# Performance work log

Hardware: AMD Instinct MI355X
Metric: run time of the kernel (lower is better)

## Reference

```python
import jax, jax.numpy as jnp
import numpy as np


def _rot_x(a):  # a: [N], angle = theta[:,1]
    c, s = jnp.cos(a), jnp.sin(a)
    z, o = jnp.zeros_like(c), jnp.ones_like(c)
    return jnp.stack([
        jnp.stack([o, z, z, z], -1),
        jnp.stack([z, c, -s, z], -1),
        jnp.stack([z, s, c, z], -1),
        jnp.stack([z, z, z, o], -1)], axis=1)  # [N,4,4]


def _rot_y(a):  # angle = theta[:,0]
    c, s = jnp.cos(a), jnp.sin(a)
    z, o = jnp.zeros_like(c), jnp.ones_like(c)
    return jnp.stack([
        jnp.stack([c, z, s, z], -1),
        jnp.stack([z, o, z, z], -1),
        jnp.stack([-s, z, c, z], -1),
        jnp.stack([z, z, z, o], -1)], axis=1)


def _rot_z(a):  # angle = theta[:,2]
    c, s = jnp.cos(a), jnp.sin(a)
    z, o = jnp.zeros_like(c), jnp.ones_like(c)
    return jnp.stack([
        jnp.stack([c, -s, z, z], -1),
        jnp.stack([s, c, z, z], -1),
        jnp.stack([z, z, o, z], -1),
        jnp.stack([z, z, z, o], -1)], axis=1)


def _trans(th):  # th: [N,6] -> [N,3,4] affine translation matrix
    tx, ty, tz = th[:, 3], th[:, 4], th[:, 5]
    z, o = jnp.zeros_like(tx), jnp.ones_like(tx)
    return jnp.stack([
        jnp.stack([o, z, z, tx], -1),
        jnp.stack([z, o, z, ty], -1),
        jnp.stack([z, z, o, tz], -1)], axis=1)  # [N,3,4]


def _homogeneous(x_flat, J):
    # x_flat: [N, 3*J] -> [N, 4, J] homogeneous coords (joints as columns)
    N = x_flat.shape[0]
    pts = x_flat.reshape(N, J, 3).transpose(0, 2, 1)  # [N,3,J]
    ones = jnp.ones((N, 1, J), dtype=x_flat.dtype)
    return jnp.concatenate([pts, ones], axis=1)  # [N,4,J]


def va_forward(conv_input, theta):
    B, T, D = conv_input.shape
    J = D // 3
    th = theta.reshape(-1, theta.shape[-1])  # [N,6], N = B*T
    mask = (conv_input != 0.0).astype(conv_input.dtype)  # [B,T,D]

    # translation: out = Trans @ hom(x)
    hom = _homogeneous(conv_input.reshape(-1, D), J)  # [N,4,J]
    out = jnp.einsum('nij,njk->nik', _trans(th), hom)  # [N,3,J]
    out = out.transpose(0, 2, 1).reshape(B, T, D)
    out = out * mask

    # rotation: M = Rz @ Ry @ Rx
    M = jnp.einsum('nij,njk->nik', _rot_z(th[:, 2]), _rot_y(th[:, 0]))
    M = jnp.einsum('nij,njk->nik', M, _rot_x(th[:, 1]))  # [N,4,4]
    hom2 = _homogeneous(out.reshape(-1, D), J)  # [N,4,J]
    out2 = jnp.einsum('nij,njk->nik', M, hom2)  # [N,4,J]
    out2 = out2.transpose(0, 2, 1)[:, :, 0:3]  # [N,J,3]
    return out2.reshape(B, T, D)


def setup_inputs() -> dict:
    key = jax.random.key(0)
    k1, k2 = jax.random.split(key)
    conv_input = jax.random.normal(k1, (2048, 300, 75), dtype=jnp.float32)
    theta = jax.random.normal(k2, (2048, 300, 6), dtype=jnp.float32)
    return {"conv_input": conv_input, "theta": theta}


def reference(conv_input, theta):
    return va_forward(conv_input, theta)
```

## Files before the change

kernel.cpp:

```cpp
#include <hip/hip_runtime.h>


constexpr int JOINTS = 25;

__global__ __launch_bounds__(256) void va_kernel(
    const float* __restrict__ conv,
    const float* __restrict__ theta,
    float* __restrict__ out,
    int total)
{
    int idx = blockIdx.x * 256 + threadIdx.x;
    if (idx >= total) return;

    unsigned row = (unsigned)idx / JOINTS;
    unsigned j   = (unsigned)idx - row * JOINTS;

    const float* th = theta + (size_t)row * 6;
    float ay = th[0], ax = th[1], az = th[2];
    float tx = th[3], ty = th[4], tz = th[5];

    float sy = __sinf(ay), cy = __cosf(ay);
    float sx = __sinf(ax), cx = __cosf(ax);
    float sz = __sinf(az), cz = __cosf(az);

    float m00 = cz * cy;
    float m01 = -sz * cx + cz * sy * sx;
    float m02 =  sz * sx + cz * sy * cx;
    float m10 = sz * cy;
    float m11 =  cz * cx + sz * sy * sx;
    float m12 = -cz * sx + sz * sy * cx;
    float m20 = -sy;
    float m21 = cy * sx;
    float m22 = cy * cx;

    const float* p = conv + (size_t)row * 75 + j * 3;
    float x = p[0], y = p[1], z = p[2];

    float qx = (x != 0.0f) ? (x + tx) : 0.0f;
    float qy = (y != 0.0f) ? (y + ty) : 0.0f;
    float qz = (z != 0.0f) ? (z + tz) : 0.0f;

    float ox = m00 * qx + m01 * qy + m02 * qz;
    float oy = m10 * qx + m11 * qy + m12 * qz;
    float oz = m20 * qx + m21 * qy + m22 * qz;

    float* o = out + (size_t)row * 75 + j * 3;
    o[0] = ox;
    o[1] = oy;
    o[2] = oz;
}

extern "C" void kernel_launch(void* const* d_in, const int* in_sizes, int n_in,
                              void* d_out, int out_size, void* d_ws, size_t ws_size,
                              hipStream_t stream) {
    const float* conv  = (const float*)d_in[0];
    const float* theta = (const float*)d_in[1];
    float* out = (float*)d_out;

    int total = out_size / 3;
    int blocks = (total + 255) / 256;
    va_kernel<<<blocks, 256, 0, stream>>>(conv, theta, out, total);
}
```

Measured before the change: 71.14 us.

## Stage rows in LDS with float4 loads and compute rotation once per row

Each block now loads 32 rows of input into shared memory with coalesced float4 reads and writes results back with float4 stores. This replaces the strided 3-float accesses per thread. Sin/cos and the rotation matrix are computed once per row by 32 threads instead of once per joint, then broadcast through shared memory. The cost is two barriers, LDS traffic, and idle threads during the parameter phase. Handling of a partial final block relies on total4 bounds and assumes the total float count is divisible by 4.

```diff
diff --git a/kernel.cpp b/kernel.cpp
--- a/kernel.cpp
+++ b/kernel.cpp
@@ -1,63 +1,95 @@
 #include <hip/hip_runtime.h>
 
 
-constexpr int JOINTS = 25;
+constexpr int JOINTS          = 25;
+constexpr int FLOATS_PER_ROW  = 75;
+constexpr int ROWS_PER_BLOCK  = 32;
+constexpr int BLOCK           = 256;
+constexpr int FLOATS_PER_BLK  = ROWS_PER_BLOCK * FLOATS_PER_ROW;
+constexpr int VEC4_PER_BLK    = FLOATS_PER_BLK / 4;
+constexpr int TASKS_PER_BLK   = ROWS_PER_BLOCK * JOINTS;
 
-__global__ __launch_bounds__(256) void va_kernel(
-    const float* __restrict__ conv,
-    const float* __restrict__ theta,
-    float* __restrict__ out,
-    int total)
+__global__ __launch_bounds__(BLOCK) void va_kernel(
+    const float4* __restrict__ conv4,
+    const float*  __restrict__ theta,
+    float4*       __restrict__ out4,
+    int nrows)
 {
-    int idx = blockIdx.x * 256 + threadIdx.x;
-    if (idx >= total) return;
+    __shared__ float buf[FLOATS_PER_BLK];
+    __shared__ float prm[ROWS_PER_BLOCK][12];
 
-    unsigned row = (unsigned)idx / JOINTS;
-    unsigned j   = (unsigned)idx - row * JOINTS;
+    const int tid = threadIdx.x;
+    const size_t row0  = (size_t)blockIdx.x * ROWS_PER_BLOCK;
+    const size_t base4 = (size_t)blockIdx.x * VEC4_PER_BLK;
+    const size_t total4 = (size_t)nrows * FLOATS_PER_ROW / 4;
 
-    const float* th = theta + (size_t)row * 6;
-    float ay = th[0], ax = th[1], az = th[2];
-    float tx = th[3], ty = th[4], tz = th[5];
+    #pragma unroll
+    for (int i = tid; i < VEC4_PER_BLK; i += BLOCK) {
+        size_t g = base4 + i;
+        if (g < total4)
+            *reinterpret_cast<float4*>(&buf[i * 4]) = conv4[g];
+    }
 
-    float sy = __sinf(ay), cy = __cosf(ay);
-    float sx = __sinf(ax), cx = __cosf(ax);
-    float sz = __sinf(az), cz = __cosf(az);
+    if (tid < ROWS_PER_BLOCK) {
+        size_t row = row0 + tid;
+        if (row < (size_t)nrows) {
+            const float* th = theta + row * 6;
+            float ay = th[0], ax = th[1], az = th[2];
+            float tx = th[3], ty = th[4], tz = th[5];
 
-    float m00 = cz * cy;
-    float m01 = -sz * cx + cz * sy * sx;
-    float m02 =  sz * sx + cz * sy * cx;
-    float m10 = sz * cy;
-    float m11 =  cz * cx + sz * sy * sx;
-    float m12 = -cz * sx + sz * sy * cx;
-    float m20 = -sy;
-    float m21 = cy * sx;
-    float m22 = cy * cx;
+            float sy = __sinf(ay), cy = __cosf(ay);
+            float sx = __sinf(ax), cx = __cosf(ax);
+            float sz = __sinf(az), cz = __cosf(az);
 
-    const float* p = conv + (size_t)row * 75 + j * 3;
-    float x = p[0], y = p[1], z = p[2];
+            prm[tid][0] = cz * cy;
+            prm[tid][1] = -sz * cx + cz * sy * sx;
+            prm[tid][2] =  sz * sx + cz * sy * cx;
+            prm[tid][3] = sz * cy;
+            prm[tid][4] =  cz * cx + sz * sy * sx;
+            prm[tid][5] = -cz * sx + sz * sy * cx;
+            prm[tid][6] = -sy;
+            prm[tid][7] = cy * sx;
+            prm[tid][8] = cy * cx;
+            prm[tid][9]  = tx;
+            prm[tid][10] = ty;
+            prm[tid][11] = tz;
+        }
+    }
+    __syncthreads();
 
-    float qx = (x != 0.0f) ? (x + tx) : 0.0f;
-    float qy = (y != 0.0f) ? (y + ty) : 0.0f;
-    float qz = (z != 0.0f) ? (z + tz) : 0.0f;
+    #pragma unroll
+    for (int t = tid; t < TASKS_PER_BLK; t += BLOCK) {
+        int r = t / JOINTS;
+        float* p = &buf[3 * t];
+        const float* m = prm[r];
 
-    float ox = m00 * qx + m01 * qy + m02 * qz;
-    float oy = m10 * qx + m11 * qy + m12 * qz;
-    float oz = m20 * qx + m21 * qy + m22 * qz;
+        float x = p[0], y = p[1], z = p[2];
+        float qx = (x != 0.0f) ? (x + m[9])  : 0.0f;
+        float qy = (y != 0.0f) ? (y + m[10]) : 0.0f;
+        float qz = (z != 0.0f) ? (z + m[11]) : 0.0f;
 
-    float* o = out + (size_t)row * 75 + j * 3;
-    o[0] = ox;
-    o[1] = oy;
-    o[2] = oz;
+        p[0] = m[0] * qx + m[1] * qy + m[2] * qz;
+        p[1] = m[3] * qx + m[4] * qy + m[5] * qz;
+        p[2] = m[6] * qx + m[7] * qy + m[8] * qz;
+    }
+    __syncthreads();
+
+    #pragma unroll
+    for (int i = tid; i < VEC4_PER_BLK; i += BLOCK) {
+        size_t g = base4 + i;
+        if (g < total4)
+            out4[g] = *reinterpret_cast<const float4*>(&buf[i * 4]);
+    }
 }
 
 extern "C" void kernel_launch(void* const* d_in, const int* in_sizes, int n_in,
                               void* d_out, int out_size, void* d_ws, size_t ws_size,
                               hipStream_t stream) {
-    const float* conv  = (const float*)d_in[0];
-    const float* theta = (const float*)d_in[1];
-    float* out = (float*)d_out;
+    const float4* conv4 = (const float4*)d_in[0];
+    const float*  theta = (const float*)d_in[1];
+    float4* out4 = (float4*)d_out;
 
-    int total = out_size / 3;
-    int blocks = (total + 255) / 256;
-    va_kernel<<<blocks, 256, 0, stream>>>(conv, theta, out, total);
+    int nrows  = out_size / FLOATS_PER_ROW;
+    int blocks = (nrows + ROWS_PER_BLOCK - 1) / ROWS_PER_BLOCK;
+    va_kernel<<<blocks, BLOCK, 0, stream>>>(conv4, theta, out4, nrows);
 }
```

Measured after the change: 77.91 us. +9.5%, slower.

## Vectorize to float4 per thread with wave shuffles for cross-joint neighbors

Applied to the files above, without the earlier changes.

Each thread now handles four consecutive output floats, loaded and stored as one 16-byte nontemporal vector. Neighbouring values needed to complete xyz triplets come from adjacent lanes via shuffles, with boundary lanes falling back to scalar loads. This replaces the stride-3 scalar accesses with fully coalesced vector traffic. The cost is that each thread computes up to two rotation matrices (six sincos) because its four floats can span two rows, plus extra select logic. The launch also assumes the element count divides evenly into blocks of 1024 floats and drops the bounds check.

```diff
diff --git a/kernel.cpp b/kernel.cpp
--- a/kernel.cpp
+++ b/kernel.cpp
@@ -1,53 +1,101 @@
 #include <hip/hip_runtime.h>
 
 
-constexpr int JOINTS = 25;
+typedef float f32x4 __attribute__((ext_vector_type(4)));
 
-__global__ __launch_bounds__(256) void va_kernel(
+constexpr int BLOCK = 256;
+
+__global__ __launch_bounds__(BLOCK) void va_kernel(
     const float* __restrict__ conv,
     const float* __restrict__ theta,
     float* __restrict__ out,
-    int total)
+    int F)
 {
-    int idx = blockIdx.x * 256 + threadIdx.x;
-    if (idx >= total) return;
+    int q = blockIdx.x * BLOCK + threadIdx.x;
+    int g = q << 2;
 
-    unsigned row = (unsigned)idx / JOINTS;
-    unsigned j   = (unsigned)idx - row * JOINTS;
+    f32x4 A = __builtin_nontemporal_load((const f32x4*)conv + q);
 
-    const float* th = theta + (size_t)row * 6;
-    float ay = th[0], ax = th[1], az = th[2];
-    float tx = th[3], ty = th[4], tz = th[5];
+    int lane = threadIdx.x & 63;
 
-    float sy = __sinf(ay), cy = __cosf(ay);
-    float sx = __sinf(ax), cx = __cosf(ax);
-    float sz = __sinf(az), cz = __cosf(az);
+    float w0 = __shfl_up(A.z, 1);
+    float w1 = __shfl_up(A.w, 1);
+    float w6 = __shfl_down(A.x, 1);
+    float w7 = __shfl_down(A.y, 1);
+    if (lane == 0) {
+        w0 = (g >= 2) ? conv[g - 2] : 0.0f;
+        w1 = (g >= 1) ? conv[g - 1] : 0.0f;
+    }
+    if (lane == 63) {
+        w6 = (g + 4 < F) ? conv[g + 4] : 0.0f;
+        w7 = (g + 5 < F) ? conv[g + 5] : 0.0f;
+    }
+    float w2 = A.x, w3 = A.y, w4 = A.z, w5 = A.w;
 
-    float m00 = cz * cy;
-    float m01 = -sz * cx + cz * sy * sx;
-    float m02 =  sz * sx + cz * sy * cx;
-    float m10 = sz * cy;
-    float m11 =  cz * cx + sz * sy * sx;
-    float m12 = -cz * sx + sz * sy * cx;
-    float m20 = -sy;
-    float m21 = cy * sx;
-    float m22 = cy * cx;
+    unsigned ug = (unsigned)g;
+    unsigned ra = ug / 75u;
+    unsigned u0 = ug - ra * 75u;
+    unsigned rb = (u0 >= 72u) ? ra + 1u : ra;
 
-    const float* p = conv + (size_t)row * 75 + j * 3;
-    float x = p[0], y = p[1], z = p[2];
+    float a00,a01,a02,a10,a11,a12,a20,a21,a22, atx,aty,atz;
+    float b00,b01,b02,b10,b11,b12,b20,b21,b22, btx,bty,btz;
+    {
+        const float* th = theta + (size_t)ra * 6;
+        float ay=th[0], ax=th[1], az=th[2]; atx=th[3]; aty=th[4]; atz=th[5];
+        float sy=__sinf(ay), cy=__cosf(ay);
+        float sx=__sinf(ax), cx=__cosf(ax);
+        float sz=__sinf(az), cz=__cosf(az);
+        a00=cz*cy; a01=-sz*cx+cz*sy*sx; a02= sz*sx+cz*sy*cx;
+        a10=sz*cy; a11= cz*cx+sz*sy*sx; a12=-cz*sx+sz*sy*cx;
+        a20=-sy;   a21=cy*sx;           a22=cy*cx;
+    }
+    {
+        const float* th = theta + (size_t)rb * 6;
+        float ay=th[0], ax=th[1], az=th[2]; btx=th[3]; bty=th[4]; btz=th[5];
+        float sy=__sinf(ay), cy=__cosf(ay);
+        float sx=__sinf(ax), cx=__cosf(ax);
+        float sz=__sinf(az), cz=__cosf(az);
+        b00=cz*cy; b01=-sz*cx+cz*sy*sx; b02= sz*sx+cz*sy*cx;
+        b10=sz*cy; b11= cz*cx+sz*sy*sx; b12=-cz*sx+sz*sy*cx;
+        b20=-sy;   b21=cy*sx;           b22=cy*cx;
+    }
 
-    float qx = (x != 0.0f) ? (x + tx) : 0.0f;
-    float qy = (y != 0.0f) ? (y + ty) : 0.0f;
-    float qz = (z != 0.0f) ? (z + tz) : 0.0f;
+    f32x4 O;
 
-    float ox = m00 * qx + m01 * qy + m02 * qz;
-    float oy = m10 * qx + m11 * qy + m12 * qz;
-    float oz = m20 * qx + m21 * qy + m22 * qz;
+#define COMP(i, v0, v1, v2, v3, v4, OUT)                                   \
+    {                                                                      \
+        unsigned ui  = u0 + (i);                                           \
+        bool     inB = ui >= 75u;                                          \
+        unsigned uu  = inB ? ui - 75u : ui;                                \
+        unsigned c   = uu - (uu / 3u) * 3u;                                \
+        float s0 = (c == 0u) ? (v2) : ((c == 1u) ? (v1) : (v0));           \
+        float s1 = (c == 0u) ? (v3) : ((c == 1u) ? (v2) : (v1));           \
+        float s2 = (c == 0u) ? (v4) : ((c == 1u) ? (v3) : (v2));           \
+        float tx = inB ? btx : atx;                                        \
+        float ty = inB ? bty : aty;                                        \
+        float tz = inB ? btz : atz;                                        \
+        float qx = (s0 != 0.0f) ? s0 + tx : 0.0f;                          \
+        float qy = (s1 != 0.0f) ? s1 + ty : 0.0f;                          \
+        float qz = (s2 != 0.0f) ? s2 + tz : 0.0f;                          \
+        float p0 = (c == 0u) ? a00 : ((c == 1u) ? a10 : a20);              \
+        float p1 = (c == 0u) ? a01 : ((c == 1u) ? a11 : a21);              \
+        float p2 = (c == 0u) ? a02 : ((c == 1u) ? a12 : a22);              \
+        float r0 = (c == 0u) ? b00 : ((c == 1u) ? b10 : b20);              \
+        float r1 = (c == 0u) ? b01 : ((c == 1u) ? b11 : b21);              \
+        float r2 = (c == 0u) ? b02 : ((c == 1u) ? b12 : b22);              \
+        float m0 = inB ? r0 : p0;                                          \
+        float m1 = inB ? r1 : p1;                                          \
+        float m2 = inB ? r2 : p2;                                          \
+        OUT = m0 * qx + m1 * qy + m2 * qz;                                 \
+    }
 
-    float* o = out + (size_t)row * 75 + j * 3;
-    o[0] = ox;
-    o[1] = oy;
-    o[2] = oz;
+    COMP(0, w0, w1, w2, w3, w4, O.x)
+    COMP(1, w1, w2, w3, w4, w5, O.y)
+    COMP(2, w2, w3, w4, w5, w6, O.z)
+    COMP(3, w3, w4, w5, w6, w7, O.w)
+#undef COMP
+
+    __builtin_nontemporal_store(O, (f32x4*)out + q);
 }
 
 extern "C" void kernel_launch(void* const* d_in, const int* in_sizes, int n_in,
@@ -57,7 +105,8 @@
     const float* theta = (const float*)d_in[1];
     float* out = (float*)d_out;
 
-    int total = out_size / 3;
-    int blocks = (total + 255) / 256;
-    va_kernel<<<blocks, 256, 0, stream>>>(conv, theta, out, total);
+    int F = out_size;
+    int nf4 = F / 4;
+    int blocks = nf4 / BLOCK;
+    va_kernel<<<blocks, BLOCK, 0, stream>>>(conv, theta, out, F);
 }
```

Result: slower. 96.65 us (+35.9%).
